# Performance work log

Measured on AMD Instinct MI355X. Metric: run time of the kernel, lower is better.

The kernel has to match this reference:

```python
import jax, jax.numpy as jnp
import numpy as np

N_NODES = 50000
N_EDGES = 800000
NUM_MOL = 2000
MSG_PASSES = 4


def setup_inputs() -> dict:
    key = jax.random.key(0)
    ks = jax.random.split(key, 16)
    x = jax.random.randint(ks[0], (N_NODES,), 0, 119)
    edge_attr = jax.random.randint(ks[1], (N_EDGES,), 0, 4)
    edge_index = jax.random.randint(ks[2], (2, N_EDGES), 0, N_NODES)
    batch = jnp.sort(jax.random.randint(ks[3], (N_NODES,), 0, NUM_MOL))
    f32 = jnp.float32
    return {
        "x": x,
        "edge_attr": edge_attr,
        "edge_index": edge_index,
        "batch": batch,
        "atom_table": jax.random.normal(ks[4], (119, 128), f32) * 0.1,
        "bond_table": jax.random.normal(ks[5], (4, 64), f32) * 0.1,
        "Wi": jax.random.normal(ks[6], (192, 128), f32) * 0.05,
        "bi": jax.random.normal(ks[7], (128,), f32) * 0.01,
        "Wu1": jax.random.normal(ks[8], (320, 128), f32) * 0.05,
        "bu1": jax.random.normal(ks[9], (128,), f32) * 0.01,
        "Wu2": jax.random.normal(ks[10], (128, 128), f32) * 0.05,
        "bu2": jax.random.normal(ks[11], (128,), f32) * 0.01,
        "Wr1": jax.random.normal(ks[12], (128, 512), f32) * 0.05,
        "br1": jax.random.normal(ks[13], (512,), f32) * 0.01,
        "Wr2": jax.random.normal(ks[14], (512, 1), f32) * 0.05,
        "br2": jax.random.normal(ks[15], (1,), f32) * 0.01,
    }


def reference(x, edge_attr, edge_index, batch,
              atom_table, bond_table, Wi, bi, Wu1, bu1, Wu2, bu2,
              Wr1, br1, Wr2, br2):
    atom = atom_table[x]                      # [N, atom_emb]
    bond = bond_table[edge_attr]              # [E, bond_emb]
    src, dst = edge_index[0], edge_index[1]
    a_src = atom[src]                         # [E, atom_emb]
    ab = jnp.concatenate([a_src, bond], axis=1)  # [E, atom_emb+bond_emb]
    msg = jax.nn.relu(ab @ Wi + bi)           # [E, msg_dim]
    for _ in range(MSG_PASSES):
        agg = jax.ops.segment_sum(msg, dst, num_segments=N_NODES)  # [N, msg_dim]
        upd_in = jnp.concatenate([ab, agg[src]], axis=1)           # [E, 320]
        h = jax.nn.relu(upd_in @ Wu1 + bu1)
        msg = jax.nn.relu(h @ Wu2 + bu2)
    node_state = jax.ops.segment_sum(msg, dst, num_segments=N_NODES)
    mol_state = jax.ops.segment_sum(node_state, batch, num_segments=NUM_MOL)
    out = jax.nn.relu(mol_state @ Wr1 + br1) @ Wr2 + br2  # [NUM_MOL, 1]
    return jnp.squeeze(out, axis=-1)
```

## Files before the change

### kernel.cpp

```cpp
#include <hip/hip_runtime.h>
#include <hip/hip_bf16.h>

#define N_NODES 50000
#define N_EDGES 800000
#define NUM_MOL 2000

typedef __attribute__((ext_vector_type(8))) short short8;
typedef __attribute__((ext_vector_type(4))) float f32x4;

union bfbits { __hip_bfloat16 b; short s; };

__global__ void k_tables(const float* __restrict__ atom_table,
                         const float* __restrict__ bond_table,
                         const float* __restrict__ Wi,
                         const float* __restrict__ bi,
                         const float* __restrict__ Wu1,
                         const float* __restrict__ bu1,
                         float* __restrict__ T1, float* __restrict__ U1,
                         float* __restrict__ T2c, float* __restrict__ U2c) {
  int b = blockIdx.x;
  int c = threadIdx.x;
  if (b < 119) {
    float t = 0.f, u = 0.f;
    for (int k = 0; k < 128; k++) {
      float a = atom_table[b * 128 + k];
      t += a * Wi[k * 128 + c];
      u += a * Wu1[k * 128 + c];
    }
    T1[b * 128 + c] = t;
    U1[b * 128 + c] = u;
  } else {
    int a = b - 119;
    float t = bi[c], u = bu1[c];
    for (int k = 0; k < 64; k++) {
      float bv = bond_table[a * 64 + k];
      t += bv * Wi[(128 + k) * 128 + c];
      u += bv * Wu1[(128 + k) * 128 + c];
    }
    T2c[a * 128 + c] = t;
    U2c[a * 128 + c] = u;
  }
}

__global__ void k_prep(const float* __restrict__ T1, const float* __restrict__ T2c,
                       const float* __restrict__ Wu2, const float* __restrict__ Wu1,
                       float* __restrict__ TT,
                       short* __restrict__ Wt, short* __restrict__ Wlo,
                       short* __restrict__ W1t, short* __restrict__ W1lo) {
  int b = blockIdx.x;
  int k = threadIdx.x;
  if (b < 476) {
    float v = T1[(b >> 2) * 128 + k] + T2c[(b & 3) * 128 + k];
    TT[b * 128 + k] = v > 0.f ? v : 0.f;
  } else if (b < 604) {
    int n = b - 476;
    float w = Wu2[k * 128 + n];
    bfbits hi; hi.b = __float2bfloat16(w);
    float hf = __bfloat162float(hi.b);
    bfbits lo; lo.b = __float2bfloat16(w - hf);
    Wt[n * 128 + k] = hi.s;
    Wlo[n * 128 + k] = lo.s;
  } else {
    int n = b - 604;
    float w = Wu1[(192 + k) * 128 + n];
    bfbits hi; hi.b = __float2bfloat16(w);
    float hf = __bfloat162float(hi.b);
    bfbits lo; lo.b = __float2bfloat16(w - hf);
    W1t[n * 128 + k] = hi.s;
    W1lo[n * 128 + k] = lo.s;
  }
}

__global__ void k_fillb(const int* __restrict__ eidx, const int* __restrict__ attr,
                        const int* __restrict__ x,
                        int* __restrict__ cnt, int* __restrict__ csr1) {
  int e = blockIdx.x * 256 + threadIdx.x;
  int d = eidx[N_EDGES + e];
  int s = eidx[e];
  int a = attr[e];
  int pos = atomicAdd(&cnt[d], 1);
  if (pos < 64) {
    int packed = (s * 4 + a) | ((x[s] * 4 + a) << 18);
    csr1[d * 64 + pos] = packed;
  }
}

__global__ void k_molptr(const int* __restrict__ batch, int* __restrict__ molptr) {
  int m = blockIdx.x * 256 + threadIdx.x;
  if (m > NUM_MOL) return;
  int lo = 0, hi = N_NODES;
  while (lo < hi) {
    int mid = (lo + hi) >> 1;
    if (batch[mid] < m) lo = mid + 1; else hi = mid;
  }
  molptr[m] = lo;
}

__global__ void k_gather0(const int* __restrict__ cnt, const int* __restrict__ csr1,
                          const float* __restrict__ TT, float* __restrict__ A_) {
  int n = blockIdx.x * 4 + (threadIdx.x >> 6);
  int lane = threadIdx.x & 63;
  int g = lane >> 5;
  int p = lane & 31;
  int beg = n * 64;
  int end = beg + cnt[n];
  float s0 = 0.f, s1 = 0.f, s2 = 0.f, s3 = 0.f;
  int i = beg;
  for (; i + 7 < end; i += 8) {
    int iA = ((unsigned)csr1[i + g]) >> 18;
    int iB = ((unsigned)csr1[i + 2 + g]) >> 18;
    int iC = ((unsigned)csr1[i + 4 + g]) >> 18;
    int iD = ((unsigned)csr1[i + 6 + g]) >> 18;
    float4 va = *(const float4*)&TT[iA * 128 + p * 4];
    float4 vb = *(const float4*)&TT[iB * 128 + p * 4];
    float4 vc = *(const float4*)&TT[iC * 128 + p * 4];
    float4 vd = *(const float4*)&TT[iD * 128 + p * 4];
    s0 += (va.x + vb.x) + (vc.x + vd.x);
    s1 += (va.y + vb.y) + (vc.y + vd.y);
    s2 += (va.z + vb.z) + (vc.z + vd.z);
    s3 += (va.w + vb.w) + (vc.w + vd.w);
  }
  for (; i + 3 < end; i += 4) {
    int iA = ((unsigned)csr1[i + g]) >> 18;
    int iB = ((unsigned)csr1[i + 2 + g]) >> 18;
    float4 va = *(const float4*)&TT[iA * 128 + p * 4];
    float4 vb = *(const float4*)&TT[iB * 128 + p * 4];
    s0 += va.x + vb.x; s1 += va.y + vb.y;
    s2 += va.z + vb.z; s3 += va.w + vb.w;
  }
  for (; i < end; i += 2) {
    if (i + g < end) {
      int idx = ((unsigned)csr1[i + g]) >> 18;
      float4 v = *(const float4*)&TT[idx * 128 + p * 4];
      s0 += v.x; s1 += v.y; s2 += v.z; s3 += v.w;
    }
  }
  s0 += __shfl_xor(s0, 32, 64);
  s1 += __shfl_xor(s1, 32, 64);
  s2 += __shfl_xor(s2, 32, 64);
  s3 += __shfl_xor(s3, 32, 64);
  float2 o;
  o.x = (g == 0) ? s0 : s2;
  o.y = (g == 0) ? s1 : s3;
  *(float2*)&A_[n * 128 + p * 4 + g * 2] = o;
}

__global__ void k_gather(const int* __restrict__ cnt, const int* __restrict__ csr1,
                         const __hip_bfloat16* __restrict__ M, float* __restrict__ A_) {
  int n = blockIdx.x * 4 + (threadIdx.x >> 6);
  int lane = threadIdx.x & 63;
  int g = lane >> 4;
  int p = lane & 15;
  int beg = n * 64;
  int end = beg + cnt[n];
  float s[8];
#pragma unroll
  for (int j = 0; j < 8; j++) s[j] = 0.f;
  const short* Ms = (const short*)M;
  int i = beg;
  for (; i + 15 < end; i += 16) {
    int iA = csr1[i + g] & 0x3FFFF;
    int iB = csr1[i + 4 + g] & 0x3FFFF;
    int iC = csr1[i + 8 + g] & 0x3FFFF;
    int iD = csr1[i + 12 + g] & 0x3FFFF;
    short8 va = *(const short8*)&Ms[iA * 128 + p * 8];
    short8 vb = *(const short8*)&Ms[iB * 128 + p * 8];
    short8 vc = *(const short8*)&Ms[iC * 128 + p * 8];
    short8 vd = *(const short8*)&Ms[iD * 128 + p * 8];
#pragma unroll
    for (int j = 0; j < 4; j++) {
      float2 fa = __bfloat1622float2(*(const __hip_bfloat162*)&((const short*)&va)[j * 2]);
      float2 fb = __bfloat1622float2(*(const __hip_bfloat162*)&((const short*)&vb)[j * 2]);
      float2 fc = __bfloat1622float2(*(const __hip_bfloat162*)&((const short*)&vc)[j * 2]);
      float2 fd = __bfloat1622float2(*(const __hip_bfloat162*)&((const short*)&vd)[j * 2]);
      s[j * 2] += (fa.x + fb.x) + (fc.x + fd.x);
      s[j * 2 + 1] += (fa.y + fb.y) + (fc.y + fd.y);
    }
  }
  for (; i + 7 < end; i += 8) {
    int iA = csr1[i + g] & 0x3FFFF;
    int iB = csr1[i + 4 + g] & 0x3FFFF;
    short8 va = *(const short8*)&Ms[iA * 128 + p * 8];
    short8 vb = *(const short8*)&Ms[iB * 128 + p * 8];
#pragma unroll
    for (int j = 0; j < 4; j++) {
      float2 fa = __bfloat1622float2(*(const __hip_bfloat162*)&((const short*)&va)[j * 2]);
      float2 fb = __bfloat1622float2(*(const __hip_bfloat162*)&((const short*)&vb)[j * 2]);
      s[j * 2] += fa.x + fb.x;
      s[j * 2 + 1] += fa.y + fb.y;
    }
  }
  for (; i < end; i += 4) {
    if (i + g < end) {
      int idx = csr1[i + g] & 0x3FFFF;
      short8 va = *(const short8*)&Ms[idx * 128 + p * 8];
#pragma unroll
      for (int j = 0; j < 4; j++) {
        float2 fa = __bfloat1622float2(*(const __hip_bfloat162*)&((const short*)&va)[j * 2]);
        s[j * 2] += fa.x;
        s[j * 2 + 1] += fa.y;
      }
    }
  }
#pragma unroll
  for (int j = 0; j < 8; j++) s[j] += __shfl_xor(s[j], 16, 64);
#pragma unroll
  for (int j = 0; j < 8; j++) s[j] += __shfl_xor(s[j], 32, 64);
  float2 o;
  o.x = s[g * 2];
  o.y = s[g * 2 + 1];
  *(float2*)&A_[n * 128 + p * 8 + g * 2] = o;
}

__global__ __launch_bounds__(256, 2) void k_mm1m(const float* __restrict__ A_,
                                                 const short* __restrict__ W1t,
                                                 const short* __restrict__ W1lo,
                                                 const int* __restrict__ x,
                                                 const float* __restrict__ U1,
                                                 float* __restrict__ B2_) {
  __shared__ float mbuf[4][16][68];
  int t = threadIdx.x;
  int lane = t & 63;
  int m = lane & 15;
  int quad = lane >> 4;
  int wslot = t >> 6;
  int w0 = blockIdx.x * 4 + wslot;
  int h = w0 & 1;

  short8 whi[4][4], wlo[4][4];
#pragma unroll
  for (int kc = 0; kc < 4; kc++)
#pragma unroll
    for (int nt = 0; nt < 4; nt++) {
      int n = h * 64 + nt * 16 + m;
      whi[kc][nt] = *(const short8*)&W1t[n * 128 + kc * 32 + quad * 8];
      wlo[kc][nt] = *(const short8*)&W1lo[n * 128 + kc * 32 + quad * 8];
    }

  for (int tid = w0; tid < 6250; tid += 4096) {
    int s = tid >> 1;
    int row = s * 16 + m;
    f32x4 acc[4];
#pragma unroll
    for (int nt = 0; nt < 4; nt++) acc[nt] = (f32x4){0.f, 0.f, 0.f, 0.f};

#pragma unroll
    for (int kc = 0; kc < 4; kc++) {
      int k0 = kc * 32 + quad * 8;
      short8 ahi, alo;
      {
        float av[8];
        *(float4*)&av[0] = *(const float4*)&A_[row * 128 + k0];
        *(float4*)&av[4] = *(const float4*)&A_[row * 128 + k0 + 4];
#pragma unroll
        for (int j = 0; j < 8; j++) {
          float hv = av[j];
          bfbits hi; hi.b = __float2bfloat16(hv);
          float hf = __bfloat162float(hi.b);
          bfbits lo; lo.b = __float2bfloat16(hv - hf);
          ahi[j] = hi.s;
          alo[j] = lo.s;
        }
      }
#pragma unroll
      for (int nt = 0; nt < 4; nt++) {
        acc[nt] = __builtin_amdgcn_mfma_f32_16x16x32_bf16(ahi, whi[kc][nt], acc[nt], 0, 0, 0);
        acc[nt] = __builtin_amdgcn_mfma_f32_16x16x32_bf16(alo, whi[kc][nt], acc[nt], 0, 0, 0);
        acc[nt] = __builtin_amdgcn_mfma_f32_16x16x32_bf16(ahi, wlo[kc][nt], acc[nt], 0, 0, 0);
      }
    }

#pragma unroll
    for (int nt = 0; nt < 4; nt++)
#pragma unroll
      for (int r = 0; r < 4; r++)
        mbuf[wslot][quad * 4 + r][nt * 16 + m] = acc[nt][r];
#pragma unroll
    for (int p = 0; p < 4; p++) {
      int c = p * 64 + lane;
      int rr = c >> 4;
      int qf = c & 15;
      int n = s * 16 + rr;
      int xn = x[n];
      float4 v = *(const float4*)&mbuf[wslot][rr][qf * 4];
      float4 d = *(const float4*)&U1[xn * 128 + h * 64 + qf * 4];
      v.x += d.x; v.y += d.y; v.z += d.z; v.w += d.w;
      *(float4*)&B2_[n * 128 + h * 64 + qf * 4] = v;
    }
  }
}

__global__ __launch_bounds__(256, 2) void k_mm2(const float* __restrict__ B2_,
                                                const float* __restrict__ U2c,
                                                const short* __restrict__ Wt,
                                                const short* __restrict__ Wlo,
                                                const float* __restrict__ bu2,
                                                __hip_bfloat16* __restrict__ M) {
  __shared__ short mbuf[4][16][40];
  int t = threadIdx.x;
  int lane = t & 63;
  int m = lane & 15;
  int quad = lane >> 4;
  int wslot = t >> 6;
  int w0 = blockIdx.x * 4 + wslot;
  int q = w0 & 3;

  short8 whi[4][2], wlo[4][2];
#pragma unroll
  for (int kc = 0; kc < 4; kc++)
#pragma unroll
    for (int nt = 0; nt < 2; nt++) {
      int n = q * 32 + nt * 16 + m;
      whi[kc][nt] = *(const short8*)&Wt[n * 128 + kc * 32 + quad * 8];
      wlo[kc][nt] = *(const short8*)&Wlo[n * 128 + kc * 32 + quad * 8];
    }
  float bias[2];
#pragma unroll
  for (int nt = 0; nt < 2; nt++) bias[nt] = bu2[q * 32 + nt * 16 + m];

  for (int tid = w0; tid < 12500; tid += 4096) {
    int s = tid >> 2;
    int row = s * 16 + m;
    f32x4 acc[4][2];
#pragma unroll
    for (int a = 0; a < 4; a++)
#pragma unroll
      for (int nt = 0; nt < 2; nt++) acc[a][nt] = (f32x4){0.f, 0.f, 0.f, 0.f};

#pragma unroll
    for (int kc = 0; kc < 4; kc++) {
      int k0 = kc * 32 + quad * 8;
      float bba[8];
      *(float4*)&bba[0] = *(const float4*)&B2_[row * 128 + k0];
      *(float4*)&bba[4] = *(const float4*)&B2_[row * 128 + k0 + 4];
#pragma unroll
      for (int a = 0; a < 4; a++) {
        float u2a[8];
        *(float4*)&u2a[0] = *(const float4*)&U2c[a * 128 + k0];
        *(float4*)&u2a[4] = *(const float4*)&U2c[a * 128 + k0 + 4];
        short8 ahi, alo;
#pragma unroll
        for (int j = 0; j < 8; j++) {
          float hv = bba[j] + u2a[j];
          hv = hv > 0.f ? hv : 0.f;
          bfbits hi; hi.b = __float2bfloat16(hv);
          float hf = __bfloat162float(hi.b);
          bfbits lo; lo.b = __float2bfloat16(hv - hf);
          ahi[j] = hi.s;
          alo[j] = lo.s;
        }
#pragma unroll
        for (int nt = 0; nt < 2; nt++) {
          acc[a][nt] = __builtin_amdgcn_mfma_f32_16x16x32_bf16(ahi, whi[kc][nt], acc[a][nt], 0, 0, 0);
          acc[a][nt] = __builtin_amdgcn_mfma_f32_16x16x32_bf16(alo, whi[kc][nt], acc[a][nt], 0, 0, 0);
          acc[a][nt] = __builtin_amdgcn_mfma_f32_16x16x32_bf16(ahi, wlo[kc][nt], acc[a][nt], 0, 0, 0);
        }
      }
    }

#pragma unroll
    for (int a = 0; a < 4; a++) {
#pragma unroll
      for (int nt = 0; nt < 2; nt++) {
#pragma unroll
        for (int r = 0; r < 4; r++) {
          float v = acc[a][nt][r] + bias[nt];
          v = v > 0.f ? v : 0.f;
          bfbits o; o.b = __float2bfloat16(v);
          mbuf[wslot][quad * 4 + r][nt * 16 + m] = o.s;
        }
      }
      {
        int rr = lane >> 2;
        int qq = lane & 3;
        int mrow = (s * 16 + rr) * 4 + a;
        short8 v = *(const short8*)&mbuf[wslot][rr][qq * 8];
        *(short8*)((short*)M + mrow * 128 + q * 32 + qq * 8) = v;
      }
    }
  }
}

__global__ void k_molgather(const float* __restrict__ A_, const int* __restrict__ molptr,
                            float* __restrict__ mol) {
  int m = blockIdx.x * 4 + (threadIdx.x >> 6);
  int lane = threadIdx.x & 63;
  int beg = molptr[m], end = molptr[m + 1];
  float ax = 0.f, ay = 0.f;
  int n = beg;
  for (; n + 1 < end; n += 2) {
    float2 v0 = *(const float2*)&A_[n * 128 + lane * 2];
    float2 v1 = *(const float2*)&A_[(n + 1) * 128 + lane * 2];
    ax += v0.x + v1.x;
    ay += v0.y + v1.y;
  }
  if (n < end) {
    float2 v0 = *(const float2*)&A_[n * 128 + lane * 2];
    ax += v0.x;
    ay += v0.y;
  }
  float2 o; o.x = ax; o.y = ay;
  *(float2*)&mol[m * 128 + lane * 2] = o;
}

__global__ __launch_bounds__(256) void k_readout(const float* __restrict__ mol,
                                                 const float* __restrict__ Wr1,
                                                 const float* __restrict__ br1,
                                                 const float* __restrict__ Wr2,
                                                 const float* __restrict__ br2,
                                                 float* __restrict__ out) {
  int m0 = blockIdx.x * 8;
  __shared__ float ms[8][128];
  __shared__ float red[32];
  int t = threadIdx.x;
  int lane = t & 63;
  int wave = t >> 6;
  for (int i = t; i < 1024; i += 256)
    ms[i >> 7][i & 127] = mol[m0 * 128 + i];
  __syncthreads();
  float part[8];
#pragma unroll
  for (int q = 0; q < 8; q++) part[q] = 0.f;
#pragma unroll
  for (int jj = 0; jj < 2; jj++) {
    int j = t + jj * 256;
    float b1 = br1[j];
    float acc[8];
#pragma unroll
    for (int q = 0; q < 8; q++) acc[q] = b1;
    for (int k = 0; k < 128; k += 4) {
      float w0 = Wr1[k * 512 + j];
      float w1 = Wr1[(k + 1) * 512 + j];
      float w2 = Wr1[(k + 2) * 512 + j];
      float w3 = Wr1[(k + 3) * 512 + j];
#pragma unroll
      for (int q = 0; q < 8; q++)
        acc[q] += ms[q][k] * w0 + ms[q][k + 1] * w1 + ms[q][k + 2] * w2 + ms[q][k + 3] * w3;
    }
    float w2v = Wr2[j];
#pragma unroll
    for (int q = 0; q < 8; q++) {
      float a = acc[q] > 0.f ? acc[q] : 0.f;
      part[q] += a * w2v;
    }
  }
#pragma unroll
  for (int q = 0; q < 8; q++) {
    float v = part[q];
    v += __shfl_xor(v, 32, 64);
    v += __shfl_xor(v, 16, 64);
    v += __shfl_xor(v, 8, 64);
    v += __shfl_xor(v, 4, 64);
    v += __shfl_xor(v, 2, 64);
    v += __shfl_xor(v, 1, 64);
    if (lane == 0) red[wave * 8 + q] = v;
  }
  __syncthreads();
  if (t < 8)
    out[m0 + t] = red[t] + red[8 + t] + red[16 + t] + red[24 + t] + br2[0];
}

extern "C" void kernel_launch(void* const* d_in, const int* in_sizes, int n_in,
                              void* d_out, int out_size, void* d_ws, size_t ws_size,
                              hipStream_t stream) {
  const int* x        = (const int*)d_in[0];
  const int* eattr    = (const int*)d_in[1];
  const int* eidx     = (const int*)d_in[2];
  const int* batch    = (const int*)d_in[3];
  const float* atom_table = (const float*)d_in[4];
  const float* bond_table = (const float*)d_in[5];
  const float* Wi  = (const float*)d_in[6];
  const float* bi  = (const float*)d_in[7];
  const float* Wu1 = (const float*)d_in[8];
  const float* bu1 = (const float*)d_in[9];
  const float* Wu2 = (const float*)d_in[10];
  const float* bu2 = (const float*)d_in[11];
  const float* Wr1 = (const float*)d_in[12];
  const float* br1 = (const float*)d_in[13];
  const float* Wr2 = (const float*)d_in[14];
  const float* br2 = (const float*)d_in[15];
  float* out = (float*)d_out;

  char* ws = (char*)d_ws;
  __hip_bfloat16* M = (__hip_bfloat16*)(ws);
  short* Wt      = (short*)(ws + 51200000);
  short* Wlo     = (short*)(ws + 51232768);
  short* W1t     = (short*)(ws + 51265536);
  short* W1lo    = (short*)(ws + 51298304);
  int*   molptr  = (int*)  (ws + 51331072);
  int*   cnt     = (int*)  (ws + 51340000);
  int*   csr1    = (int*)  (ws + 52000000);
  float* A       = (float*)(ws + 102400000);
  float* B2      = (float*)(ws + 128000000);
  float* T1      = (float*)(ws + 157000064);
  float* U1      = (float*)(ws + 157060992);
  float* T2c     = (float*)(ws + 157121920);
  float* U2c     = (float*)(ws + 157123968);
  float* TT      = (float*)(ws + 157126016);
  float* mol     = (float*)(ws + 157369728);

  hipMemsetAsync(cnt, 0, N_NODES * sizeof(int), stream);
  k_tables<<<123, 128, 0, stream>>>(atom_table, bond_table, Wi, bi, Wu1, bu1,
                                    T1, U1, T2c, U2c);
  k_prep<<<732, 128, 0, stream>>>(T1, T2c, Wu2, Wu1, TT, Wt, Wlo, W1t, W1lo);
  k_fillb<<<N_EDGES / 256, 256, 0, stream>>>(eidx, eattr, x, cnt, csr1);
  k_molptr<<<(NUM_MOL + 256) / 256, 256, 0, stream>>>(batch, molptr);

  k_gather0<<<N_NODES / 4, 256, 0, stream>>>(cnt, csr1, TT, A);

  for (int p = 0; p < 4; p++) {
    k_mm1m<<<1024, 256, 0, stream>>>(A, W1t, W1lo, x, U1, B2);
    k_mm2<<<1024, 256, 0, stream>>>(B2, U2c, Wt, Wlo, bu2, M);
    k_gather<<<N_NODES / 4, 256, 0, stream>>>(cnt, csr1, M, A);
  }

  k_molgather<<<NUM_MOL / 4, 256, 0, stream>>>(A, molptr, mol);
  k_readout<<<NUM_MOL / 8, 256, 0, stream>>>(mol, Wr1, br1, Wr2, br2, out);
}
```

Baseline: 623.2 us.

## Fuse node-level first matmul into message matmul kernel via shared-memory staging

Merges the two per-pass matmul kernels into one. Each block computes a 16-node tile of A·W1 (each wave covering 32 output columns) and writes it to a double-buffered shared-memory tile. After a block barrier it adds U1[x] and runs the second matmul over the four bond variants. This removes the B2 global round trip and one kernel launch per pass. In exchange each wave keeps both weight sets in registers at occupancy 1, and every tile needs a block-wide barrier.

```diff
diff --git a/kernel.cpp b/kernel.cpp
--- a/kernel.cpp
+++ b/kernel.cpp
@@ -212,127 +212,96 @@
   *(float2*)&A_[n * 128 + p * 8 + g * 2] = o;
 }
 
-__global__ __launch_bounds__(256, 2) void k_mm1m(const float* __restrict__ A_,
-                                                 const short* __restrict__ W1t,
-                                                 const short* __restrict__ W1lo,
-                                                 const int* __restrict__ x,
-                                                 const float* __restrict__ U1,
-                                                 float* __restrict__ B2_) {
-  __shared__ float mbuf[4][16][68];
-  int t = threadIdx.x;
-  int lane = t & 63;
-  int m = lane & 15;
-  int quad = lane >> 4;
-  int wslot = t >> 6;
-  int w0 = blockIdx.x * 4 + wslot;
-  int h = w0 & 1;
-
-  short8 whi[4][4], wlo[4][4];
-#pragma unroll
-  for (int kc = 0; kc < 4; kc++)
-#pragma unroll
-    for (int nt = 0; nt < 4; nt++) {
-      int n = h * 64 + nt * 16 + m;
-      whi[kc][nt] = *(const short8*)&W1t[n * 128 + kc * 32 + quad * 8];
-      wlo[kc][nt] = *(const short8*)&W1lo[n * 128 + kc * 32 + quad * 8];
-    }
-
-  for (int tid = w0; tid < 6250; tid += 4096) {
-    int s = tid >> 1;
-    int row = s * 16 + m;
-    f32x4 acc[4];
-#pragma unroll
-    for (int nt = 0; nt < 4; nt++) acc[nt] = (f32x4){0.f, 0.f, 0.f, 0.f};
-
-#pragma unroll
-    for (int kc = 0; kc < 4; kc++) {
-      int k0 = kc * 32 + quad * 8;
-      short8 ahi, alo;
-      {
-        float av[8];
-        *(float4*)&av[0] = *(const float4*)&A_[row * 128 + k0];
-        *(float4*)&av[4] = *(const float4*)&A_[row * 128 + k0 + 4];
-#pragma unroll
-        for (int j = 0; j < 8; j++) {
-          float hv = av[j];
-          bfbits hi; hi.b = __float2bfloat16(hv);
-          float hf = __bfloat162float(hi.b);
-          bfbits lo; lo.b = __float2bfloat16(hv - hf);
-          ahi[j] = hi.s;
-          alo[j] = lo.s;
-        }
-      }
-#pragma unroll
-      for (int nt = 0; nt < 4; nt++) {
-        acc[nt] = __builtin_amdgcn_mfma_f32_16x16x32_bf16(ahi, whi[kc][nt], acc[nt], 0, 0, 0);
-        acc[nt] = __builtin_amdgcn_mfma_f32_16x16x32_bf16(alo, whi[kc][nt], acc[nt], 0, 0, 0);
-        acc[nt] = __builtin_amdgcn_mfma_f32_16x16x32_bf16(ahi, wlo[kc][nt], acc[nt], 0, 0, 0);
-      }
-    }
-
-#pragma unroll
-    for (int nt = 0; nt < 4; nt++)
-#pragma unroll
-      for (int r = 0; r < 4; r++)
-        mbuf[wslot][quad * 4 + r][nt * 16 + m] = acc[nt][r];
-#pragma unroll
-    for (int p = 0; p < 4; p++) {
-      int c = p * 64 + lane;
-      int rr = c >> 4;
-      int qf = c & 15;
-      int n = s * 16 + rr;
-      int xn = x[n];
-      float4 v = *(const float4*)&mbuf[wslot][rr][qf * 4];
-      float4 d = *(const float4*)&U1[xn * 128 + h * 64 + qf * 4];
-      v.x += d.x; v.y += d.y; v.z += d.z; v.w += d.w;
-      *(float4*)&B2_[n * 128 + h * 64 + qf * 4] = v;
-    }
-  }
-}
-
-__global__ __launch_bounds__(256, 2) void k_mm2(const float* __restrict__ B2_,
-                                                const float* __restrict__ U2c,
+__global__ __launch_bounds__(256, 1) void k_mmf(const float* __restrict__ A_,
+                                                const short* __restrict__ W1t,
+                                                const short* __restrict__ W1lo,
                                                 const short* __restrict__ Wt,
                                                 const short* __restrict__ Wlo,
+                                                const int* __restrict__ x,
+                                                const float* __restrict__ U1,
+                                                const float* __restrict__ U2c,
                                                 const float* __restrict__ bu2,
                                                 __hip_bfloat16* __restrict__ M) {
+  __shared__ float b2s[2][16][132];
   __shared__ short mbuf[4][16][40];
   int t = threadIdx.x;
   int lane = t & 63;
   int m = lane & 15;
   int quad = lane >> 4;
   int wslot = t >> 6;
-  int w0 = blockIdx.x * 4 + wslot;
-  int q = w0 & 3;
-
-  short8 whi[4][2], wlo[4][2];
+  int q = wslot;
+
+  short8 w1hi[4][2], w1lo[4][2], w2hi[4][2], w2lo[4][2];
 #pragma unroll
   for (int kc = 0; kc < 4; kc++)
 #pragma unroll
     for (int nt = 0; nt < 2; nt++) {
       int n = q * 32 + nt * 16 + m;
-      whi[kc][nt] = *(const short8*)&Wt[n * 128 + kc * 32 + quad * 8];
-      wlo[kc][nt] = *(const short8*)&Wlo[n * 128 + kc * 32 + quad * 8];
+      w1hi[kc][nt] = *(const short8*)&W1t[n * 128 + kc * 32 + quad * 8];
+      w1lo[kc][nt] = *(const short8*)&W1lo[n * 128 + kc * 32 + quad * 8];
+      w2hi[kc][nt] = *(const short8*)&Wt[n * 128 + kc * 32 + quad * 8];
+      w2lo[kc][nt] = *(const short8*)&Wlo[n * 128 + kc * 32 + quad * 8];
     }
   float bias[2];
 #pragma unroll
   for (int nt = 0; nt < 2; nt++) bias[nt] = bu2[q * 32 + nt * 16 + m];
 
-  for (int tid = w0; tid < 12500; tid += 4096) {
-    int s = tid >> 2;
+  int buf = 0;
+  for (int s = blockIdx.x; s < 3125; s += gridDim.x) {
     int row = s * 16 + m;
-    f32x4 acc[4][2];
+
+    f32x4 acc1[2];
+#pragma unroll
+    for (int nt = 0; nt < 2; nt++) acc1[nt] = (f32x4){0.f, 0.f, 0.f, 0.f};
+#pragma unroll
+    for (int kc = 0; kc < 4; kc++) {
+      int k0 = kc * 32 + quad * 8;
+      float av[8];
+      *(float4*)&av[0] = *(const float4*)&A_[row * 128 + k0];
+      *(float4*)&av[4] = *(const float4*)&A_[row * 128 + k0 + 4];
+      short8 ahi, alo;
+#pragma unroll
+      for (int j = 0; j < 8; j++) {
+        float hv = av[j];
+        bfbits hi; hi.b = __float2bfloat16(hv);
+        float hf = __bfloat162float(hi.b);
+        bfbits lo; lo.b = __float2bfloat16(hv - hf);
+        ahi[j] = hi.s;
+        alo[j] = lo.s;
+      }
+#pragma unroll
+      for (int nt = 0; nt < 2; nt++) {
+        acc1[nt] = __builtin_amdgcn_mfma_f32_16x16x32_bf16(ahi, w1hi[kc][nt], acc1[nt], 0, 0, 0);
+        acc1[nt] = __builtin_amdgcn_mfma_f32_16x16x32_bf16(alo, w1hi[kc][nt], acc1[nt], 0, 0, 0);
+        acc1[nt] = __builtin_amdgcn_mfma_f32_16x16x32_bf16(ahi, w1lo[kc][nt], acc1[nt], 0, 0, 0);
+      }
+    }
+#pragma unroll
+    for (int nt = 0; nt < 2; nt++)
+#pragma unroll
+      for (int r = 0; r < 4; r++)
+        b2s[buf][quad * 4 + r][q * 32 + nt * 16 + m] = acc1[nt][r];
+
+    __syncthreads();
+
+    int xn = x[row];
+    f32x4 acc2[4][2];
 #pragma unroll
     for (int a = 0; a < 4; a++)
 #pragma unroll
-      for (int nt = 0; nt < 2; nt++) acc[a][nt] = (f32x4){0.f, 0.f, 0.f, 0.f};
+      for (int nt = 0; nt < 2; nt++) acc2[a][nt] = (f32x4){0.f, 0.f, 0.f, 0.f};
 
 #pragma unroll
     for (int kc = 0; kc < 4; kc++) {
       int k0 = kc * 32 + quad * 8;
       float bba[8];
-      *(float4*)&bba[0] = *(const float4*)&B2_[row * 128 + k0];
-      *(float4*)&bba[4] = *(const float4*)&B2_[row * 128 + k0 + 4];
+      {
+        float u1v[8];
+        *(float4*)&u1v[0] = *(const float4*)&U1[xn * 128 + k0];
+        *(float4*)&u1v[4] = *(const float4*)&U1[xn * 128 + k0 + 4];
+#pragma unroll
+        for (int j = 0; j < 8; j++) bba[j] = b2s[buf][m][k0 + j] + u1v[j];
+      }
 #pragma unroll
       for (int a = 0; a < 4; a++) {
         float u2a[8];
@@ -351,9 +320,9 @@
         }
 #pragma unroll
         for (int nt = 0; nt < 2; nt++) {
-          acc[a][nt] = __builtin_amdgcn_mfma_f32_16x16x32_bf16(ahi, whi[kc][nt], acc[a][nt], 0, 0, 0);
-          acc[a][nt] = __builtin_amdgcn_mfma_f32_16x16x32_bf16(alo, whi[kc][nt], acc[a][nt], 0, 0, 0);
-          acc[a][nt] = __builtin_amdgcn_mfma_f32_16x16x32_bf16(ahi, wlo[kc][nt], acc[a][nt], 0, 0, 0);
+          acc2[a][nt] = __builtin_amdgcn_mfma_f32_16x16x32_bf16(ahi, w2hi[kc][nt], acc2[a][nt], 0, 0, 0);
+          acc2[a][nt] = __builtin_amdgcn_mfma_f32_16x16x32_bf16(alo, w2hi[kc][nt], acc2[a][nt], 0, 0, 0);
+          acc2[a][nt] = __builtin_amdgcn_mfma_f32_16x16x32_bf16(ahi, w2lo[kc][nt], acc2[a][nt], 0, 0, 0);
         }
       }
     }
@@ -364,7 +333,7 @@
       for (int nt = 0; nt < 2; nt++) {
 #pragma unroll
         for (int r = 0; r < 4; r++) {
-          float v = acc[a][nt][r] + bias[nt];
+          float v = acc2[a][nt][r] + bias[nt];
           v = v > 0.f ? v : 0.f;
           bfbits o; o.b = __float2bfloat16(v);
           mbuf[wslot][quad * 4 + r][nt * 16 + m] = o.s;
@@ -378,6 +347,7 @@
         *(short8*)((short*)M + mrow * 128 + q * 32 + qq * 8) = v;
       }
     }
+    buf ^= 1;
   }
 }
 
@@ -491,7 +461,6 @@
   int*   cnt     = (int*)  (ws + 51340000);
   int*   csr1    = (int*)  (ws + 52000000);
   float* A       = (float*)(ws + 102400000);
-  float* B2      = (float*)(ws + 128000000);
   float* T1      = (float*)(ws + 157000064);
   float* U1      = (float*)(ws + 157060992);
   float* T2c     = (float*)(ws + 157121920);
@@ -509,8 +478,7 @@
   k_gather0<<<N_NODES / 4, 256, 0, stream>>>(cnt, csr1, TT, A);
 
   for (int p = 0; p < 4; p++) {
-    k_mm1m<<<1024, 256, 0, stream>>>(A, W1t, W1lo, x, U1, B2);
-    k_mm2<<<1024, 256, 0, stream>>>(B2, U2c, Wt, Wlo, bu2, M);
+    k_mmf<<<1024, 256, 0, stream>>>(A, W1t, W1lo, Wt, Wlo, x, U1, U2c, bu2, M);
     k_gather<<<N_NODES / 4, 256, 0, stream>>>(cnt, csr1, M, A);
   }
 
```

After: 661.6 us. 1.06x slower.
